# Performance work log

Measured on AMD Instinct MI355X. Metric: run time of the kernel, lower is better.

Reference implementation:

```python
import jax, jax.numpy as jnp
import numpy as np

B, Md, L, SHOTS, UP = 8, 256, 31, 2, 2  # batch, downsampled spatial, bands, shots, upsample factor


def setup_inputs() -> dict:
    key = jax.random.key(0)
    k1, k2 = jax.random.split(key)
    Y = jax.random.uniform(k1, (B, Md, Md + L - 1, SHOTS), dtype=jnp.float32)
    H = jax.random.uniform(k2, (B, Md, Md, L, SHOTS), dtype=jnp.float32)
    return {"Y": Y, "H": H}


def reference(Y, H):
    # CASSI adjoint: X[b,m,n,l,s] = Y[b,m,(n+l) mod N2,s]  (tf.roll(-l) + slice [0:Md])
    N2 = Y.shape[2]  # Md + L - 1
    idx = (jnp.arange(Md)[:, None] + jnp.arange(L)[None, :]) % N2  # (Md, L)
    X = Y[:, :, idx, :]                      # (B, Md, Md, L, SHOTS) gather
    X = jnp.sum(H * X, axis=4)               # mask multiply + sum over shots -> (B, Md, Md, L)
    X = X / jnp.max(X)                        # global-max normalization
    # UpSampling2D(size=(2,2)), nearest, channels_last
    X = jnp.repeat(jnp.repeat(X, UP, axis=1), UP, axis=2)  # (B, 2*Md, 2*Md, L)
    return X
```

## Files before the change

### kernel.cpp

```cpp
#include <hip/hip_runtime.h>

#define NPAIR 8126464u

typedef float vfloat4 __attribute__((ext_vector_type(4)));

__global__ __launch_bounds__(256) void k_max(
    const float4* __restrict__ H4, const float2* __restrict__ Y2,
    int* __restrict__ maxslot)
{
    float m = 0.0f;
    const unsigned stride = gridDim.x * blockDim.x;
    for (unsigned p = blockIdx.x * blockDim.x + threadIdx.x; p < NPAIR; p += stride) {
        unsigned e0 = 2u * p, e1 = e0 + 1u;
        unsigned q0 = e0 / 31u, l0 = e0 - q0 * 31u;
        unsigned q1 = e1 / 31u, l1 = e1 - q1 * 31u;
        unsigned y0 = (q0 >> 8) * 286u + (q0 & 255u) + l0;
        unsigned y1 = (q1 >> 8) * 286u + (q1 & 255u) + l1;
        float4 h = H4[p];
        float2 ya = Y2[y0], yb = Y2[y1];
        m = fmaxf(m, fmaxf(h.x * ya.x + h.y * ya.y, h.z * yb.x + h.w * yb.y));
    }
    #pragma unroll
    for (int off = 32; off > 0; off >>= 1)
        m = fmaxf(m, __shfl_xor(m, off, 64));
    __shared__ float wmax[4];
    const int lane = threadIdx.x & 63, wid = threadIdx.x >> 6;
    if (lane == 0) wmax[wid] = m;
    __syncthreads();
    if (threadIdx.x == 0) {
        float bmax = fmaxf(fmaxf(wmax[0], wmax[1]), fmaxf(wmax[2], wmax[3]));
        atomicMax(maxslot, __float_as_int(bmax));
    }
}

__global__ __launch_bounds__(256) void k_out(
    const float4* __restrict__ H4, const float2* __restrict__ Y2,
    const int* __restrict__ maxslot, vfloat4* __restrict__ out4)
{
    __shared__ float xs[992];
    const unsigned bm = blockIdx.x >> 3;
    const unsigned ti = blockIdx.x & 7u;
    const float inv = 1.0f / __int_as_float(*maxslot);

    const unsigned h4base = bm * 3968u + ti * 496u;
    const unsigned ybase  = bm * 286u + ti * 32u;
    for (unsigned f2 = threadIdx.x; f2 < 496u; f2 += 256u) {
        unsigned f  = 2u * f2;
        unsigned c0 = f / 31u,        l0 = f        - c0 * 31u;
        unsigned c1 = (f + 1u) / 31u, l1 = (f + 1u) - c1 * 31u;
        float4 h  = H4[h4base + f2];
        float2 ya = Y2[ybase + c0 + l0];
        float2 yb = Y2[ybase + c1 + l1];
        xs[f]      = h.x * ya.x + h.y * ya.y;
        xs[f + 1u] = h.z * yb.x + h.w * yb.y;
    }
    __syncthreads();

    const unsigned b = bm >> 8, mrow = bm & 255u;
    vfloat4* r0 = out4 + (size_t)((b * 512u + 2u * mrow) * 3968u + ti * 496u);
    vfloat4* r1 = r0 + 3968u;
    for (unsigned g = threadIdx.x; g < 496u; g += 256u) {
        vfloat4 v;
        #pragma unroll
        for (int k = 0; k < 4; ++k) {
            unsigned s  = 4u * g + (unsigned)k;
            unsigned oc = s / 31u, r = s - oc * 31u;
            v[k] = xs[(oc >> 1) * 31u + r] * inv;
        }
        __builtin_nontemporal_store(v, &r0[g]);
        __builtin_nontemporal_store(v, &r1[g]);
    }
}

extern "C" void kernel_launch(void* const* d_in, const int* in_sizes, int n_in,
                              void* d_out, int out_size, void* d_ws, size_t ws_size,
                              hipStream_t stream) {
    const float* Y = (const float*)d_in[0];
    const float* H = (const float*)d_in[1];

    int* maxslot = (int*)d_ws;

    k_max<<<2048, 256, 0, stream>>>((const float4*)H, (const float2*)Y, maxslot);
    k_out<<<8 * 256 * 8, 256, 0, stream>>>((const float4*)H, (const float2*)Y,
                                           maxslot, (vfloat4*)d_out);
}
```

Measured before the change: 373.9 us.

## Materialize shot-summed X in the max pass and reuse it in the upsample pass

The max-reduction kernel now also writes the shot-summed product H*Y to a workspace buffer. The output kernel then reads that compact buffer instead of re-reading the full H tensor and re-doing the Y gather and multiply. This removes the second pass over H, at the cost of an extra write and read of an intermediate half H's size. It also relies on the workspace being large enough to hold that intermediate.

```diff
diff --git a/kernel.cpp b/kernel.cpp
--- a/kernel.cpp
+++ b/kernel.cpp
@@ -4,9 +4,9 @@
 
 typedef float vfloat4 __attribute__((ext_vector_type(4)));
 
-__global__ __launch_bounds__(256) void k_max(
+__global__ __launch_bounds__(256) void k_maxX(
     const float4* __restrict__ H4, const float2* __restrict__ Y2,
-    int* __restrict__ maxslot)
+    int* __restrict__ maxslot, float2* __restrict__ X2)
 {
     float m = 0.0f;
     const unsigned stride = gridDim.x * blockDim.x;
@@ -18,7 +18,10 @@
         unsigned y1 = (q1 >> 8) * 286u + (q1 & 255u) + l1;
         float4 h = H4[p];
         float2 ya = Y2[y0], yb = Y2[y1];
-        m = fmaxf(m, fmaxf(h.x * ya.x + h.y * ya.y, h.z * yb.x + h.w * yb.y));
+        float xa = h.x * ya.x + h.y * ya.y;
+        float xb = h.z * yb.x + h.w * yb.y;
+        X2[p] = make_float2(xa, xb);
+        m = fmaxf(m, fmaxf(xa, xb));
     }
     #pragma unroll
     for (int off = 32; off > 0; off >>= 1)
@@ -33,39 +36,27 @@
     }
 }
 
-__global__ __launch_bounds__(256) void k_out(
-    const float4* __restrict__ H4, const float2* __restrict__ Y2,
-    const int* __restrict__ maxslot, vfloat4* __restrict__ out4)
+__global__ __launch_bounds__(256) void k_out2(
+    const float* __restrict__ X, const int* __restrict__ maxslot,
+    vfloat4* __restrict__ out4)
 {
-    __shared__ float xs[992];
     const unsigned bm = blockIdx.x >> 3;
     const unsigned ti = blockIdx.x & 7u;
     const float inv = 1.0f / __int_as_float(*maxslot);
+    const float* __restrict__ Xr = X + bm * 7936u;
 
-    const unsigned h4base = bm * 3968u + ti * 496u;
-    const unsigned ybase  = bm * 286u + ti * 32u;
-    for (unsigned f2 = threadIdx.x; f2 < 496u; f2 += 256u) {
-        unsigned f  = 2u * f2;
-        unsigned c0 = f / 31u,        l0 = f        - c0 * 31u;
-        unsigned c1 = (f + 1u) / 31u, l1 = (f + 1u) - c1 * 31u;
-        float4 h  = H4[h4base + f2];
-        float2 ya = Y2[ybase + c0 + l0];
-        float2 yb = Y2[ybase + c1 + l1];
-        xs[f]      = h.x * ya.x + h.y * ya.y;
-        xs[f + 1u] = h.z * yb.x + h.w * yb.y;
-    }
-    __syncthreads();
+    vfloat4* r0 = out4 + (size_t)((bm >> 8) * 512u + 2u * (bm & 255u)) * 3968u
+                       + ti * 496u;
+    vfloat4* r1 = r0 + 3968u;
 
-    const unsigned b = bm >> 8, mrow = bm & 255u;
-    vfloat4* r0 = out4 + (size_t)((b * 512u + 2u * mrow) * 3968u + ti * 496u);
-    vfloat4* r1 = r0 + 3968u;
     for (unsigned g = threadIdx.x; g < 496u; g += 256u) {
+        const unsigned sbase = (ti * 496u + g) * 4u;
         vfloat4 v;
         #pragma unroll
         for (int k = 0; k < 4; ++k) {
-            unsigned s  = 4u * g + (unsigned)k;
+            unsigned s  = sbase + (unsigned)k;
             unsigned oc = s / 31u, r = s - oc * 31u;
-            v[k] = xs[(oc >> 1) * 31u + r] * inv;
+            v[k] = Xr[(oc >> 1) * 31u + r] * inv;
         }
         __builtin_nontemporal_store(v, &r0[g]);
         __builtin_nontemporal_store(v, &r1[g]);
@@ -79,8 +70,10 @@
     const float* H = (const float*)d_in[1];
 
     int* maxslot = (int*)d_ws;
+    float2* X2   = (float2*)((char*)d_ws + 256);
 
-    k_max<<<2048, 256, 0, stream>>>((const float4*)H, (const float2*)Y, maxslot);
-    k_out<<<8 * 256 * 8, 256, 0, stream>>>((const float4*)H, (const float2*)Y,
-                                           maxslot, (vfloat4*)d_out);
+    k_maxX<<<2048, 256, 0, stream>>>((const float4*)H, (const float2*)Y,
+                                     maxslot, X2);
+    k_out2<<<8 * 256 * 8, 256, 0, stream>>>((const float*)X2, maxslot,
+                                            (vfloat4*)d_out);
 }
```

Result: no change. 367.0 us (-1.8%).
